# Kernel optimization log

Measured on AMD Instinct MI355X. Metric: run time of the kernel, lower is better.

The kernel has to match this reference:

```python
import jax, jax.numpy as jnp
import numpy as np

# pywt Wavelet('db4') decomposition filters (8 taps)
DB4_DEC_LO = np.array([-0.010597401784997278, 0.032883011666982945,
                       0.030841381835986965, -0.18703481171888114,
                       -0.027983769416983849, 0.63088076792959036,
                       0.71484657055254153, 0.23037781330885523], dtype=np.float32)
# quadrature mirror: dec_hi[k] = (-1)^(k+1) * dec_lo[F-1-k]
DB4_DEC_HI = (DB4_DEC_LO[::-1] * np.array([-1.0, 1.0] * 4, dtype=np.float32)).astype(np.float32)
LEVELS = 4


def _dwt_step(x, lo, hi):
    """One pywt.dwt level, mode='symmetric'. x: [B, L] -> (cA, cD) each [B, floor((L+F-1)/2)]."""
    F = lo.shape[0]
    # symmetric half-sample extension by F-1 on each side, then drop one sample so a
    # stride-2 VALID correlation picks the odd-indexed outputs of the full valid conv
    ext = jnp.pad(x, ((0, 0), (F - 1, F - 1)), mode='symmetric')[:, 1:]
    inp = ext[:, None, :]                                # [B, 1, Lext]
    # pywt convolves (flipped filter); lax conv is correlation, so flip filters here
    ker = jnp.stack([lo[::-1], hi[::-1]])[:, None, :]    # [2, 1, F]
    y = jax.lax.conv_general_dilated(inp, ker, window_strides=(2,), padding='VALID',
                                     dimension_numbers=('NCH', 'OIH', 'NCH'))
    return y[:, 0, :], y[:, 1, :]


def _wavedec(x, levels):
    lo = jnp.asarray(DB4_DEC_LO)
    hi = jnp.asarray(DB4_DEC_HI)
    details = []
    ca = x
    for _ in range(levels):
        ca, cd = _dwt_step(ca, lo, hi)
        details.append(cd)
    # pywt ordering: [cA_n, cD_n, cD_{n-1}, ..., cD_1]
    return [ca] + details[::-1]


def setup_inputs() -> dict:
    key = jax.random.key(0)
    kx, kw, kb = jax.random.split(key, 3)
    B, L = 4096, 4096
    x = jax.random.normal(kx, (B, L), dtype=jnp.float32)
    weights = jax.random.normal(kw, (LEVELS + 1, 1), dtype=jnp.float32)
    bias = jax.random.normal(kb, (LEVELS + 1, 1), dtype=jnp.float32)
    return {"x": x, "weights": weights, "bias": bias}


def reference(x, weights, bias):
    coeffs = _wavedec(x, LEVELS)
    # per-band learnable affine: coeff_j * w_j + b_j (w_j, b_j scalars broadcast over [B, L_j])
    out = tuple(c * weights[j, 0] + bias[j, 0] for j, c in enumerate(coeffs))
    return out
```

## Files before the change

kernel.cpp:

```cpp
#include <hip/hip_runtime.h>

#define NT 256

#define L0 -0.010597401784997278f
#define L1f 0.032883011666982945f
#define L2f 0.030841381835986965f
#define L3f -0.18703481171888114f
#define L4f -0.02798376941698385f
#define L5f 0.6308807679295904f
#define L6f 0.7148465705525415f
#define L7f 0.23037781330885523f


constexpr int B_ROWS = 4096;
constexpr int LVL1 = 4096, N1 = 2051, N2 = 1029, N3 = 518, N4 = 262;
constexpr size_t OFF_CA4 = 0;
constexpr size_t OFF_CD4 = (size_t)B_ROWS * N4;
constexpr size_t OFF_CD3 = OFF_CD4 + (size_t)B_ROWS * N4;
constexpr size_t OFF_CD2 = OFF_CD3 + (size_t)B_ROWS * N3;
constexpr size_t OFF_CD1 = OFF_CD2 + (size_t)B_ROWS * N2;

__device__ __forceinline__ void dwt_one_clamped(const float* __restrict__ src, int L, int t,
                                                float& slo, float& shi) {
    constexpr float LOR[8] = {L7f, L6f, L5f, L4f, L3f, L2f, L1f, L0};
    constexpr float HIR[8] = {L0, -L1f, L2f, -L3f, L4f, -L5f, L6f, -L7f};
    const int idx0 = 2 * t - 6;
    slo = 0.f; shi = 0.f;
#pragma unroll
    for (int m = 0; m < 8; ++m) {
        int q = idx0 + m;
        q = (q < 0) ? (-1 - q) : q;
        q = (q >= L) ? (2 * L - 1 - q) : q;
        const float v = src[q];
        slo = fmaf(LOR[m], v, slo);
        shi = fmaf(HIR[m], v, shi);
    }
}

template <bool SCALE_A>
__device__ __forceinline__ void dwt_level_blk(const float* __restrict__ src, int L,
                                              float* __restrict__ dstA, float wa, float ba,
                                              float* __restrict__ outD, float wd, float bd) {
    constexpr float LOR[8] = {L7f, L6f, L5f, L4f, L3f, L2f, L1f, L0};
    constexpr float HIR[8] = {L0, -L1f, L2f, -L3f, L4f, -L5f, L6f, -L7f};
    const int N = (L + 7) >> 1;
    const int Mmax = (L - 8) >> 3;
    const int tid = threadIdx.x;

    const float h0 = wd * HIR[0], h1 = wd * HIR[1], h2 = wd * HIR[2], h3 = wd * HIR[3],
                h4 = wd * HIR[4], h5 = wd * HIR[5], h6 = wd * HIR[6], h7 = wd * HIR[7];
    const float g0 = wa * LOR[0], g1 = wa * LOR[1], g2 = wa * LOR[2], g3 = wa * LOR[3],
                g4 = wa * LOR[4], g5 = wa * LOR[5], g6 = wa * LOR[6], g7 = wa * LOR[7];

    for (int m = 1 + tid; m <= Mmax; m += NT) {
        const float4* p = reinterpret_cast<const float4*>(src) + (2 * m - 2);
        const float4 v0 = p[0], v1 = p[1], v2 = p[2], v3 = p[3];
        const float W[16] = {v0.x, v0.y, v0.z, v0.w, v1.x, v1.y, v1.z, v1.w,
                             v2.x, v2.y, v2.z, v2.w, v3.x, v3.y, v3.z, v3.w};
        float accA[4], accD[4];
#pragma unroll
        for (int o = 0; o < 4; ++o) {
            float sd = bd;
            sd = fmaf(h0, W[2 * o + 2], sd);
            sd = fmaf(h1, W[2 * o + 3], sd);
            sd = fmaf(h2, W[2 * o + 4], sd);
            sd = fmaf(h3, W[2 * o + 5], sd);
            sd = fmaf(h4, W[2 * o + 6], sd);
            sd = fmaf(h5, W[2 * o + 7], sd);
            sd = fmaf(h6, W[2 * o + 8], sd);
            sd = fmaf(h7, W[2 * o + 9], sd);
            accD[o] = sd;
            float sa;
            if (SCALE_A) {
                sa = ba;
                sa = fmaf(g0, W[2 * o + 2], sa);
                sa = fmaf(g1, W[2 * o + 3], sa);
                sa = fmaf(g2, W[2 * o + 4], sa);
                sa = fmaf(g3, W[2 * o + 5], sa);
                sa = fmaf(g4, W[2 * o + 6], sa);
                sa = fmaf(g5, W[2 * o + 7], sa);
                sa = fmaf(g6, W[2 * o + 8], sa);
                sa = fmaf(g7, W[2 * o + 9], sa);
            } else {
                sa = LOR[0] * W[2 * o + 2];
                sa = fmaf(LOR[1], W[2 * o + 3], sa);
                sa = fmaf(LOR[2], W[2 * o + 4], sa);
                sa = fmaf(LOR[3], W[2 * o + 5], sa);
                sa = fmaf(LOR[4], W[2 * o + 6], sa);
                sa = fmaf(LOR[5], W[2 * o + 7], sa);
                sa = fmaf(LOR[6], W[2 * o + 8], sa);
                sa = fmaf(LOR[7], W[2 * o + 9], sa);
            }
            accA[o] = sa;
        }
        const int t0 = 4 * m;
        if (SCALE_A) {
            dstA[t0 + 0] = accA[0]; dstA[t0 + 1] = accA[1];
            dstA[t0 + 2] = accA[2]; dstA[t0 + 3] = accA[3];
        } else {
            float4 qa; qa.x = accA[0]; qa.y = accA[1]; qa.z = accA[2]; qa.w = accA[3];
            *(reinterpret_cast<float4*>(dstA) + m) = qa;
        }
        outD[t0 + 0] = accD[0]; outD[t0 + 1] = accD[1];
        outD[t0 + 2] = accD[2]; outD[t0 + 3] = accD[3];
    }

    const int NS = N - 4 * Mmax;
    if (tid < NS) {
        const int t = (tid < 4) ? tid : (4 * Mmax + tid);
        float slo, shi;
        dwt_one_clamped(src, L, t, slo, shi);
        dstA[t] = SCALE_A ? fmaf(wa, slo, ba) : slo;
        outD[t] = fmaf(wd, shi, bd);
    }
}

__global__ __launch_bounds__(NT) void lwt_kernel(const float* __restrict__ x,
                                                 const float* __restrict__ w,
                                                 const float* __restrict__ bias,
                                                 float* __restrict__ out) {
    __shared__ __align__(16) float P[N1];
    __shared__ __align__(16) float Q[N2];
    const int row = blockIdx.x;
    const int tid = threadIdx.x;
    const float* __restrict__ xr = x + (size_t)row * LVL1;

    const float w0 = w[0], w1 = w[1], w2 = w[2], w3 = w[3], w4 = w[4];
    const float b0 = bias[0], b1 = bias[1], b2 = bias[2], b3 = bias[3], b4 = bias[4];

    float* outCD1 = out + OFF_CD1 + (size_t)row * N1;
    float* outCD2 = out + OFF_CD2 + (size_t)row * N2;
    float* outCD3 = out + OFF_CD3 + (size_t)row * N3;
    float* outCD4 = out + OFF_CD4 + (size_t)row * N4;
    float* outCA4 = out + OFF_CA4 + (size_t)row * N4;

    {
        constexpr float LOR[8] = {L7f, L6f, L5f, L4f, L3f, L2f, L1f, L0};
        constexpr float HIR[8] = {L0, -L1f, L2f, -L3f, L4f, -L5f, L6f, -L7f};
        const float h0 = w4 * HIR[0], h1 = w4 * HIR[1], h2 = w4 * HIR[2], h3 = w4 * HIR[3],
                    h4 = w4 * HIR[4], h5 = w4 * HIR[5], h6 = w4 * HIR[6], h7 = w4 * HIR[7];
        for (int m = 1 + tid; m <= 511; m += NT) {
            const float4* p = reinterpret_cast<const float4*>(xr) + (2 * m - 2);
            const float4 v0 = p[0], v1 = p[1], v2 = p[2], v3 = p[3];
            const float W[16] = {v0.x, v0.y, v0.z, v0.w, v1.x, v1.y, v1.z, v1.w,
                                 v2.x, v2.y, v2.z, v2.w, v3.x, v3.y, v3.z, v3.w};
            float accA[4], accD[4];
#pragma unroll
            for (int o = 0; o < 4; ++o) {
                float sd = b4;
                sd = fmaf(h0, W[2 * o + 2], sd);
                sd = fmaf(h1, W[2 * o + 3], sd);
                sd = fmaf(h2, W[2 * o + 4], sd);
                sd = fmaf(h3, W[2 * o + 5], sd);
                sd = fmaf(h4, W[2 * o + 6], sd);
                sd = fmaf(h5, W[2 * o + 7], sd);
                sd = fmaf(h6, W[2 * o + 8], sd);
                sd = fmaf(h7, W[2 * o + 9], sd);
                accD[o] = sd;
                float sa = LOR[0] * W[2 * o + 2];
                sa = fmaf(LOR[1], W[2 * o + 3], sa);
                sa = fmaf(LOR[2], W[2 * o + 4], sa);
                sa = fmaf(LOR[3], W[2 * o + 5], sa);
                sa = fmaf(LOR[4], W[2 * o + 6], sa);
                sa = fmaf(LOR[5], W[2 * o + 7], sa);
                sa = fmaf(LOR[6], W[2 * o + 8], sa);
                sa = fmaf(LOR[7], W[2 * o + 9], sa);
                accA[o] = sa;
            }
            const int t0 = 4 * m;
            float4 qa; qa.x = accA[0]; qa.y = accA[1]; qa.z = accA[2]; qa.w = accA[3];
            *(reinterpret_cast<float4*>(P) + m) = qa;
            outCD1[t0 + 0] = accD[0]; outCD1[t0 + 1] = accD[1];
            outCD1[t0 + 2] = accD[2]; outCD1[t0 + 3] = accD[3];
        }
        if (tid < 7) {
            const int t = (tid < 4) ? tid : (2044 + tid);
            float slo, shi;
            dwt_one_clamped(xr, LVL1, t, slo, shi);
            P[t] = slo;
            outCD1[t] = fmaf(w4, shi, b4);
        }
    }

    __syncthreads();
    dwt_level_blk<false>(P, N1, Q, 0.f, 0.f, outCD2, w3, b3);
    __syncthreads();
    dwt_level_blk<false>(Q, N2, P, 0.f, 0.f, outCD3, w2, b2);
    __syncthreads();
    dwt_level_blk<true>(P, N3, outCA4, w0, b0, outCD4, w1, b1);
}

extern "C" void kernel_launch(void* const* d_in, const int* in_sizes, int n_in,
                              void* d_out, int out_size, void* d_ws, size_t ws_size,
                              hipStream_t stream) {
    const float* x = (const float*)d_in[0];
    const float* wp = (const float*)d_in[1];
    const float* bp = (const float*)d_in[2];
    float* out = (float*)d_out;
    lwt_kernel<<<dim3(B_ROWS), dim3(NT), 0, stream>>>(x, wp, bp, out);
}
```

Baseline: 27.69 us.

## Software-pipeline level-1 DWT of next row with levels 2-4 of previous row

```diff
diff --git a/kernel.cpp b/kernel.cpp
--- a/kernel.cpp
+++ b/kernel.cpp
@@ -1,6 +1,7 @@
 #include <hip/hip_runtime.h>
 
 #define NT 256
+#define R_PB 4
 
 #define L0 -0.010597401784997278f
 #define L1f 0.032883011666982945f
@@ -115,79 +116,110 @@
     }
 }
 
+__device__ __forceinline__ void l1_window(const float4& v0, const float4& v1,
+                                          const float4& v2, const float4& v3,
+                                          int m, float* __restrict__ Pn,
+                                          float* __restrict__ cd1,
+                                          float w4, float b4) {
+    constexpr float LOR[8] = {L7f, L6f, L5f, L4f, L3f, L2f, L1f, L0};
+    constexpr float HIR[8] = {L0, -L1f, L2f, -L3f, L4f, -L5f, L6f, -L7f};
+    const float W[16] = {v0.x, v0.y, v0.z, v0.w, v1.x, v1.y, v1.z, v1.w,
+                         v2.x, v2.y, v2.z, v2.w, v3.x, v3.y, v3.z, v3.w};
+    float accA[4], accD[4];
+#pragma unroll
+    for (int o = 0; o < 4; ++o) {
+        float sd = HIR[0] * W[2 * o + 2];
+        float sa = LOR[0] * W[2 * o + 2];
+#pragma unroll
+        for (int mm = 1; mm < 8; ++mm) {
+            sd = fmaf(HIR[mm], W[2 * o + mm + 2], sd);
+            sa = fmaf(LOR[mm], W[2 * o + mm + 2], sa);
+        }
+        accD[o] = fmaf(w4, sd, b4);
+        accA[o] = sa;
+    }
+    float4 qa; qa.x = accA[0]; qa.y = accA[1]; qa.z = accA[2]; qa.w = accA[3];
+    *(reinterpret_cast<float4*>(Pn) + m) = qa;
+    const int t0 = 4 * m;
+    cd1[t0 + 0] = accD[0]; cd1[t0 + 1] = accD[1];
+    cd1[t0 + 2] = accD[2]; cd1[t0 + 3] = accD[3];
+}
+
 __global__ __launch_bounds__(NT) void lwt_kernel(const float* __restrict__ x,
                                                  const float* __restrict__ w,
                                                  const float* __restrict__ bias,
                                                  float* __restrict__ out) {
-    __shared__ __align__(16) float P[N1];
+    __shared__ __align__(16) float P[2][N1];
     __shared__ __align__(16) float Q[N2];
-    const int row = blockIdx.x;
     const int tid = threadIdx.x;
-    const float* __restrict__ xr = x + (size_t)row * LVL1;
+    const int row0 = blockIdx.x * R_PB;
 
     const float w0 = w[0], w1 = w[1], w2 = w[2], w3 = w[3], w4 = w[4];
     const float b0 = bias[0], b1 = bias[1], b2 = bias[2], b3 = bias[3], b4 = bias[4];
 
-    float* outCD1 = out + OFF_CD1 + (size_t)row * N1;
-    float* outCD2 = out + OFF_CD2 + (size_t)row * N2;
-    float* outCD3 = out + OFF_CD3 + (size_t)row * N3;
-    float* outCD4 = out + OFF_CD4 + (size_t)row * N4;
-    float* outCA4 = out + OFF_CA4 + (size_t)row * N4;
-
-    {
-        constexpr float LOR[8] = {L7f, L6f, L5f, L4f, L3f, L2f, L1f, L0};
-        constexpr float HIR[8] = {L0, -L1f, L2f, -L3f, L4f, -L5f, L6f, -L7f};
-        const float h0 = w4 * HIR[0], h1 = w4 * HIR[1], h2 = w4 * HIR[2], h3 = w4 * HIR[3],
-                    h4 = w4 * HIR[4], h5 = w4 * HIR[5], h6 = w4 * HIR[6], h7 = w4 * HIR[7];
-        for (int m = 1 + tid; m <= 511; m += NT) {
-            const float4* p = reinterpret_cast<const float4*>(xr) + (2 * m - 2);
-            const float4 v0 = p[0], v1 = p[1], v2 = p[2], v3 = p[3];
-            const float W[16] = {v0.x, v0.y, v0.z, v0.w, v1.x, v1.y, v1.z, v1.w,
-                                 v2.x, v2.y, v2.z, v2.w, v3.x, v3.y, v3.z, v3.w};
-            float accA[4], accD[4];
-#pragma unroll
-            for (int o = 0; o < 4; ++o) {
-                float sd = b4;
-                sd = fmaf(h0, W[2 * o + 2], sd);
-                sd = fmaf(h1, W[2 * o + 3], sd);
-                sd = fmaf(h2, W[2 * o + 4], sd);
-                sd = fmaf(h3, W[2 * o + 5], sd);
-                sd = fmaf(h4, W[2 * o + 6], sd);
-                sd = fmaf(h5, W[2 * o + 7], sd);
-                sd = fmaf(h6, W[2 * o + 8], sd);
-                sd = fmaf(h7, W[2 * o + 9], sd);
-                accD[o] = sd;
-                float sa = LOR[0] * W[2 * o + 2];
-                sa = fmaf(LOR[1], W[2 * o + 3], sa);
-                sa = fmaf(LOR[2], W[2 * o + 4], sa);
-                sa = fmaf(LOR[3], W[2 * o + 5], sa);
-                sa = fmaf(LOR[4], W[2 * o + 6], sa);
-                sa = fmaf(LOR[5], W[2 * o + 7], sa);
-                sa = fmaf(LOR[6], W[2 * o + 8], sa);
-                sa = fmaf(LOR[7], W[2 * o + 9], sa);
-                accA[o] = sa;
-            }
-            const int t0 = 4 * m;
-            float4 qa; qa.x = accA[0]; qa.y = accA[1]; qa.z = accA[2]; qa.w = accA[3];
-            *(reinterpret_cast<float4*>(P) + m) = qa;
-            outCD1[t0 + 0] = accD[0]; outCD1[t0 + 1] = accD[1];
-            outCD1[t0 + 2] = accD[2]; outCD1[t0 + 3] = accD[3];
-        }
-        if (tid < 7) {
-            const int t = (tid < 4) ? tid : (2044 + tid);
-            float slo, shi;
-            dwt_one_clamped(xr, LVL1, t, slo, shi);
-            P[t] = slo;
-            outCD1[t] = fmaf(w4, shi, b4);
-        }
-    }
-
-    __syncthreads();
-    dwt_level_blk<false>(P, N1, Q, 0.f, 0.f, outCD2, w3, b3);
-    __syncthreads();
-    dwt_level_blk<false>(Q, N2, P, 0.f, 0.f, outCD3, w2, b2);
-    __syncthreads();
-    dwt_level_blk<true>(P, N3, outCA4, w0, b0, outCD4, w1, b1);
+    for (int j = 0; j <= R_PB; ++j) {
+        const bool doL1 = (j < R_PB);
+        const bool doC  = (j > 0);
+        const int rowN = row0 + j;
+        const int rowC = row0 + j - 1;
+        float* Pn = P[j & 1];
+        float* Pc = P[(j & 1) ^ 1];
+        const float* xr = x + (size_t)rowN * LVL1;
+        float* cd1 = out + OFF_CD1 + (size_t)rowN * N1;
+
+        {
+            const int m = 1 + tid;
+            const bool act = doL1 && (m <= 245);
+            float4 v0, v1, v2, v3;
+            if (act) {
+                const float4* p = reinterpret_cast<const float4*>(xr) + (2 * m - 2);
+                v0 = p[0]; v1 = p[1]; v2 = p[2]; v3 = p[3];
+            }
+            if (doC)
+                dwt_level_blk<false>(Pc, N1, Q, 0.f, 0.f,
+                                     out + OFF_CD2 + (size_t)rowC * N2, w3, b3);
+            if (act) l1_window(v0, v1, v2, v3, m, Pn, cd1, w4, b4);
+        }
+        __syncthreads();
+
+        {
+            const int m = 246 + tid;
+            const bool act = doL1 && (m <= 367);
+            float4 v0, v1, v2, v3;
+            if (act) {
+                const float4* p = reinterpret_cast<const float4*>(xr) + (2 * m - 2);
+                v0 = p[0]; v1 = p[1]; v2 = p[2]; v3 = p[3];
+            }
+            if (doC)
+                dwt_level_blk<false>(Q, N2, Pc, 0.f, 0.f,
+                                     out + OFF_CD3 + (size_t)rowC * N3, w2, b2);
+            if (act) l1_window(v0, v1, v2, v3, m, Pn, cd1, w4, b4);
+        }
+        __syncthreads();
+
+        {
+            const int m = 368 + tid;
+            const bool act = doL1 && (m <= 511);
+            float4 v0, v1, v2, v3;
+            if (act) {
+                const float4* p = reinterpret_cast<const float4*>(xr) + (2 * m - 2);
+                v0 = p[0]; v1 = p[1]; v2 = p[2]; v3 = p[3];
+            }
+            if (doC)
+                dwt_level_blk<true>(Pc, N3,
+                                    out + OFF_CA4 + (size_t)rowC * N4, w0, b0,
+                                    out + OFF_CD4 + (size_t)rowC * N4, w1, b1);
+            if (act) l1_window(v0, v1, v2, v3, m, Pn, cd1, w4, b4);
+            if (doL1 && tid < 7) {
+                const int t = (tid < 4) ? tid : (2044 + tid);
+                float slo, shi;
+                dwt_one_clamped(xr, LVL1, t, slo, shi);
+                Pn[t] = slo;
+                cd1[t] = fmaf(w4, shi, b4);
+            }
+        }
+        __syncthreads();
+    }
 }
 
 extern "C" void kernel_launch(void* const* d_in, const int* in_sizes, int n_in,
@@ -197,5 +229,5 @@
     const float* wp = (const float*)d_in[1];
     const float* bp = (const float*)d_in[2];
     float* out = (float*)d_out;
-    lwt_kernel<<<dim3(B_ROWS), dim3(NT), 0, stream>>>(x, wp, bp, out);
-}
+    lwt_kernel<<<dim3(B_ROWS / R_PB), dim3(NT), 0, stream>>>(x, wp, bp, out);
+}
```

After: 40.67 us. +46.9%, slower.

## Split DWT into level-1 kernel writing workspace and levels 2-4 kernel

Applied to the files above, without the earlier changes.

```diff
diff --git a/kernel.cpp b/kernel.cpp
--- a/kernel.cpp
+++ b/kernel.cpp
@@ -19,6 +19,7 @@
 constexpr size_t OFF_CD3 = OFF_CD4 + (size_t)B_ROWS * N4;
 constexpr size_t OFF_CD2 = OFF_CD3 + (size_t)B_ROWS * N3;
 constexpr size_t OFF_CD1 = OFF_CD2 + (size_t)B_ROWS * N2;
+constexpr int WS_STRIDE = 2052;
 
 __device__ __forceinline__ void dwt_one_clamped(const float* __restrict__ src, int L, int t,
                                                 float& slo, float& shi) {
@@ -115,31 +116,27 @@
     }
 }
 
-__global__ __launch_bounds__(NT) void lwt_kernel(const float* __restrict__ x,
-                                                 const float* __restrict__ w,
-                                                 const float* __restrict__ bias,
-                                                 float* __restrict__ out) {
-    __shared__ __align__(16) float P[N1];
-    __shared__ __align__(16) float Q[N2];
+__global__ __launch_bounds__(NT) void lwt_l1_kernel(const float* __restrict__ x,
+                                                    const float* __restrict__ w,
+                                                    const float* __restrict__ bias,
+                                                    float* __restrict__ out,
+                                                    float* __restrict__ ws) {
+    constexpr float LOR[8] = {L7f, L6f, L5f, L4f, L3f, L2f, L1f, L0};
+    constexpr float HIR[8] = {L0, -L1f, L2f, -L3f, L4f, -L5f, L6f, -L7f};
     const int row = blockIdx.x;
     const int tid = threadIdx.x;
     const float* __restrict__ xr = x + (size_t)row * LVL1;
-
-    const float w0 = w[0], w1 = w[1], w2 = w[2], w3 = w[3], w4 = w[4];
-    const float b0 = bias[0], b1 = bias[1], b2 = bias[2], b3 = bias[3], b4 = bias[4];
-
-    float* outCD1 = out + OFF_CD1 + (size_t)row * N1;
-    float* outCD2 = out + OFF_CD2 + (size_t)row * N2;
-    float* outCD3 = out + OFF_CD3 + (size_t)row * N3;
-    float* outCD4 = out + OFF_CD4 + (size_t)row * N4;
-    float* outCA4 = out + OFF_CA4 + (size_t)row * N4;
-
-    {
-        constexpr float LOR[8] = {L7f, L6f, L5f, L4f, L3f, L2f, L1f, L0};
-        constexpr float HIR[8] = {L0, -L1f, L2f, -L3f, L4f, -L5f, L6f, -L7f};
-        const float h0 = w4 * HIR[0], h1 = w4 * HIR[1], h2 = w4 * HIR[2], h3 = w4 * HIR[3],
-                    h4 = w4 * HIR[4], h5 = w4 * HIR[5], h6 = w4 * HIR[6], h7 = w4 * HIR[7];
-        for (int m = 1 + tid; m <= 511; m += NT) {
+    float* __restrict__ cd1 = out + OFF_CD1 + (size_t)row * N1;
+    float* __restrict__ ca1 = ws + (size_t)row * WS_STRIDE;
+
+    const float w4 = w[4], b4 = bias[4];
+    const float h0 = w4 * HIR[0], h1 = w4 * HIR[1], h2 = w4 * HIR[2], h3 = w4 * HIR[3],
+                h4 = w4 * HIR[4], h5 = w4 * HIR[5], h6 = w4 * HIR[6], h7 = w4 * HIR[7];
+
+#pragma unroll
+    for (int it = 0; it < 2; ++it) {
+        const int m = 1 + tid + it * NT;
+        if (m <= 511) {
             const float4* p = reinterpret_cast<const float4*>(xr) + (2 * m - 2);
             const float4 v0 = p[0], v1 = p[1], v2 = p[2], v3 = p[3];
             const float W[16] = {v0.x, v0.y, v0.z, v0.w, v1.x, v1.y, v1.z, v1.w,
@@ -148,6 +145,14 @@
 #pragma unroll
             for (int o = 0; o < 4; ++o) {
                 float sd = b4;
+                float sa = LOR[0] * W[2 * o + 2];
+                sd = fmaf(h0, W[2 * o + 2], sd);
+#pragma unroll
+                for (int mm = 1; mm < 8; ++mm) {
+                    sd = fmaf((&h0)[0] * 0.f +
+                              0.f, 0.f, sd);
+                }
+                sd = b4;
                 sd = fmaf(h0, W[2 * o + 2], sd);
                 sd = fmaf(h1, W[2 * o + 3], sd);
                 sd = fmaf(h2, W[2 * o + 4], sd);
@@ -156,8 +161,7 @@
                 sd = fmaf(h5, W[2 * o + 7], sd);
                 sd = fmaf(h6, W[2 * o + 8], sd);
                 sd = fmaf(h7, W[2 * o + 9], sd);
-                accD[o] = sd;
-                float sa = LOR[0] * W[2 * o + 2];
+                sa = LOR[0] * W[2 * o + 2];
                 sa = fmaf(LOR[1], W[2 * o + 3], sa);
                 sa = fmaf(LOR[2], W[2 * o + 4], sa);
                 sa = fmaf(LOR[3], W[2 * o + 5], sa);
@@ -165,29 +169,115 @@
                 sa = fmaf(LOR[5], W[2 * o + 7], sa);
                 sa = fmaf(LOR[6], W[2 * o + 8], sa);
                 sa = fmaf(LOR[7], W[2 * o + 9], sa);
+                accD[o] = sd;
                 accA[o] = sa;
             }
             const int t0 = 4 * m;
             float4 qa; qa.x = accA[0]; qa.y = accA[1]; qa.z = accA[2]; qa.w = accA[3];
-            *(reinterpret_cast<float4*>(P) + m) = qa;
-            outCD1[t0 + 0] = accD[0]; outCD1[t0 + 1] = accD[1];
-            outCD1[t0 + 2] = accD[2]; outCD1[t0 + 3] = accD[3];
-        }
-        if (tid < 7) {
-            const int t = (tid < 4) ? tid : (2044 + tid);
-            float slo, shi;
-            dwt_one_clamped(xr, LVL1, t, slo, shi);
-            P[t] = slo;
-            outCD1[t] = fmaf(w4, shi, b4);
-        }
-    }
-
-    __syncthreads();
-    dwt_level_blk<false>(P, N1, Q, 0.f, 0.f, outCD2, w3, b3);
-    __syncthreads();
-    dwt_level_blk<false>(Q, N2, P, 0.f, 0.f, outCD3, w2, b2);
-    __syncthreads();
-    dwt_level_blk<true>(P, N3, outCA4, w0, b0, outCD4, w1, b1);
+            *reinterpret_cast<float4*>(ca1 + t0) = qa;
+            cd1[t0 + 0] = accD[0]; cd1[t0 + 1] = accD[1];
+            cd1[t0 + 2] = accD[2]; cd1[t0 + 3] = accD[3];
+        }
+    }
+    if (tid < 7) {
+        const int t = (tid < 4) ? tid : (2044 + tid);
+        float slo, shi;
+        dwt_one_clamped(xr, LVL1, t, slo, shi);
+        ca1[t] = slo;
+        cd1[t] = fmaf(w4, shi, b4);
+    }
+}
+
+__global__ __launch_bounds__(NT) void lwt_l234_kernel(const float* __restrict__ ws,
+                                                      const float* __restrict__ w,
+                                                      const float* __restrict__ bias,
+                                                      float* __restrict__ out) {
+    __shared__ __align__(16) float Q[1032];
+    __shared__ __align__(16) float R[520];
+    const int row = blockIdx.x;
+
+    const float w0 = w[0], w1 = w[1], w2 = w[2], w3 = w[3];
+    const float b0 = bias[0], b1 = bias[1], b2 = bias[2], b3 = bias[3];
+
+    const float* __restrict__ ca1 = ws + (size_t)row * WS_STRIDE;
+    float* outCD2 = out + OFF_CD2 + (size_t)row * N2;
+    float* outCD3 = out + OFF_CD3 + (size_t)row * N3;
+    float* outCD4 = out + OFF_CD4 + (size_t)row * N4;
+    float* outCA4 = out + OFF_CA4 + (size_t)row * N4;
+
+    dwt_level_blk<false>(ca1, N1, Q, 0.f, 0.f, outCD2, w3, b3);
+    __syncthreads();
+    dwt_level_blk<false>(Q, N2, R, 0.f, 0.f, outCD3, w2, b2);
+    __syncthreads();
+    dwt_level_blk<true>(R, N3, outCA4, w0, b0, outCD4, w1, b1);
+}
+
+__global__ __launch_bounds__(NT) void lwt_mono_kernel(const float* __restrict__ x,
+                                                      const float* __restrict__ w,
+                                                      const float* __restrict__ bias,
+                                                      float* __restrict__ out) {
+    __shared__ __align__(16) float P[N1];
+    __shared__ __align__(16) float Q[N2];
+    constexpr float LOR[8] = {L7f, L6f, L5f, L4f, L3f, L2f, L1f, L0};
+    constexpr float HIR[8] = {L0, -L1f, L2f, -L3f, L4f, -L5f, L6f, -L7f};
+    const int row = blockIdx.x;
+    const int tid = threadIdx.x;
+    const float* __restrict__ xr = x + (size_t)row * LVL1;
+
+    const float w0 = w[0], w1 = w[1], w2 = w[2], w3 = w[3], w4 = w[4];
+    const float b0 = bias[0], b1 = bias[1], b2 = bias[2], b3 = bias[3], b4 = bias[4];
+
+    float* outCD1 = out + OFF_CD1 + (size_t)row * N1;
+    const float h0 = w4 * HIR[0], h1 = w4 * HIR[1], h2 = w4 * HIR[2], h3 = w4 * HIR[3],
+                h4 = w4 * HIR[4], h5 = w4 * HIR[5], h6 = w4 * HIR[6], h7 = w4 * HIR[7];
+    for (int m = 1 + tid; m <= 511; m += NT) {
+        const float4* p = reinterpret_cast<const float4*>(xr) + (2 * m - 2);
+        const float4 v0 = p[0], v1 = p[1], v2 = p[2], v3 = p[3];
+        const float W[16] = {v0.x, v0.y, v0.z, v0.w, v1.x, v1.y, v1.z, v1.w,
+                             v2.x, v2.y, v2.z, v2.w, v3.x, v3.y, v3.z, v3.w};
+        float accA[4], accD[4];
+#pragma unroll
+        for (int o = 0; o < 4; ++o) {
+            float sd = b4;
+            sd = fmaf(h0, W[2 * o + 2], sd);
+            sd = fmaf(h1, W[2 * o + 3], sd);
+            sd = fmaf(h2, W[2 * o + 4], sd);
+            sd = fmaf(h3, W[2 * o + 5], sd);
+            sd = fmaf(h4, W[2 * o + 6], sd);
+            sd = fmaf(h5, W[2 * o + 7], sd);
+            sd = fmaf(h6, W[2 * o + 8], sd);
+            sd = fmaf(h7, W[2 * o + 9], sd);
+            accD[o] = sd;
+            float sa = LOR[0] * W[2 * o + 2];
+            sa = fmaf(LOR[1], W[2 * o + 3], sa);
+            sa = fmaf(LOR[2], W[2 * o + 4], sa);
+            sa = fmaf(LOR[3], W[2 * o + 5], sa);
+            sa = fmaf(LOR[4], W[2 * o + 6], sa);
+            sa = fmaf(LOR[5], W[2 * o + 7], sa);
+            sa = fmaf(LOR[6], W[2 * o + 8], sa);
+            sa = fmaf(LOR[7], W[2 * o + 9], sa);
+            accA[o] = sa;
+        }
+        const int t0 = 4 * m;
+        float4 qa; qa.x = accA[0]; qa.y = accA[1]; qa.z = accA[2]; qa.w = accA[3];
+        *(reinterpret_cast<float4*>(P) + m) = qa;
+        outCD1[t0 + 0] = accD[0]; outCD1[t0 + 1] = accD[1];
+        outCD1[t0 + 2] = accD[2]; outCD1[t0 + 3] = accD[3];
+    }
+    if (tid < 7) {
+        const int t = (tid < 4) ? tid : (2044 + tid);
+        float slo, shi;
+        dwt_one_clamped(xr, LVL1, t, slo, shi);
+        P[t] = slo;
+        outCD1[t] = fmaf(w4, shi, b4);
+    }
+    __syncthreads();
+    dwt_level_blk<false>(P, N1, Q, 0.f, 0.f, out + OFF_CD2 + (size_t)row * N2, w3, b3);
+    __syncthreads();
+    dwt_level_blk<false>(Q, N2, P, 0.f, 0.f, out + OFF_CD3 + (size_t)row * N3, w2, b2);
+    __syncthreads();
+    dwt_level_blk<true>(P, N3, out + OFF_CA4 + (size_t)row * N4, w0, b0,
+                        out + OFF_CD4 + (size_t)row * N4, w1, b1);
 }
 
 extern "C" void kernel_launch(void* const* d_in, const int* in_sizes, int n_in,
@@ -197,5 +287,12 @@
     const float* wp = (const float*)d_in[1];
     const float* bp = (const float*)d_in[2];
     float* out = (float*)d_out;
-    lwt_kernel<<<dim3(B_ROWS), dim3(NT), 0, stream>>>(x, wp, bp, out);
-}
+    const size_t need = (size_t)B_ROWS * WS_STRIDE * sizeof(float);
+    if (ws_size >= need) {
+        float* ws = (float*)d_ws;
+        lwt_l1_kernel<<<dim3(B_ROWS), dim3(NT), 0, stream>>>(x, wp, bp, out, ws);
+        lwt_l234_kernel<<<dim3(B_ROWS), dim3(NT), 0, stream>>>(ws, wp, bp, out);
+    } else {
+        lwt_mono_kernel<<<dim3(B_ROWS), dim3(NT), 0, stream>>>(x, wp, bp, out);
+    }
+}
```

Result: slower. 39.14 us (+41.4%).
